# Optimization experiments

Measured on AMD Instinct MI355X. Metric: run time of the kernel, lower is better.

The kernel has to match this reference:

```python
import jax, jax.numpy as jnp
import numpy as np


def setup_inputs() -> dict:
    key = jax.random.key(0)
    k1, k2, k3, k4 = jax.random.split(key, 4)
    B, C, H, W = 16, 256, 128, 128
    HID = 256
    in_feat_map = jax.random.normal(k1, (B, C, H, W), dtype=jnp.float32)
    act_mask = jax.random.randint(k2, (B, 1, H, W), 0, 2).astype(jnp.bool_)
    W1 = jax.random.normal(k3, (C, HID), dtype=jnp.float32) * (1.0 / np.sqrt(C))
    b1 = jnp.zeros((HID,), dtype=jnp.float32)
    W2 = jax.random.normal(k4, (HID, C), dtype=jnp.float32) * (1.0 / np.sqrt(HID))
    b2 = jnp.zeros((C,), dtype=jnp.float32)
    return {"in_feat_map": in_feat_map, "act_mask": act_mask,
            "W1": W1, "b1": b1, "W2": W2, "b2": b2}


def reference(in_feat_map, act_mask, W1, b1, W2, b2):
    # act_mask: [B,1,H,W] -> [B,H,W]. Original gathers active positions,
    # runs a pointwise MLP on [num_act, C] features, scatters back into a
    # clone. Since the inner module is pointwise per position, this equals
    # computing the MLP everywhere and selecting with the mask (same math,
    # static shapes, jit-friendly).
    mask = act_mask[:, 0]  # [B,H,W]
    # per-position 2-layer MLP over channel dim
    h = jnp.einsum('bchw,cd->bdhw', in_feat_map, W1) + b1[None, :, None, None]
    h = jax.nn.relu(h)
    y = jnp.einsum('bdhw,dc->bchw', h, W2) + b2[None, :, None, None]
    out_feat_map = jnp.where(mask[:, None, :, :], y, in_feat_map)
    return out_feat_map
```

## Files before the change

kernel.cpp:

```cpp
#include <hip/hip_runtime.h>

typedef _Float16 h4 __attribute__((ext_vector_type(4)));
typedef _Float16 h8 __attribute__((ext_vector_type(8)));
typedef float f4 __attribute__((ext_vector_type(4)));

#define CIN 256
#define HID 256
#define HWSZ 16384
#define NT 64

__global__ __launch_bounds__(256) void wconv_kernel(const float* __restrict__ W1,
                                                    const float* __restrict__ W2,
                                                    _Float16* __restrict__ W1f,
                                                    _Float16* __restrict__ W2f) {
  int t = blockIdx.x * 256 + threadIdx.x;
  int m = t & 255;
  int k = t >> 8;
  int fi = ((k >> 5) << 13) | ((m >> 4) << 9) | (((k >> 3) & 3) << 7) |
           ((m & 15) << 3) | (k & 7);
  W1f[fi] = (_Float16)W1[k * 256 + m];
  W2f[fi] = (_Float16)W2[k * 256 + m];
}

__global__ __launch_bounds__(256, 2) void mlp_kernel(
    const float* __restrict__ in, const int* __restrict__ mask,
    const float* __restrict__ b1, const float* __restrict__ b2,
    const _Float16* __restrict__ W1f, const _Float16* __restrict__ W2f,
    float* __restrict__ out) {
  __shared__ alignas(16) _Float16 Xs[NT * 256];
  __shared__ alignas(16) _Float16 Hs[NT * 256];

  const int t = threadIdx.x;
  const int g = blockIdx.x;
  const int b = g >> 8;
  const int hw0 = (g & 255) * NT;
  const float* inb = in + (size_t)b * CIN * HWSZ + hw0;

  {
    const int n = t & 63;
    const int cg = (t >> 6) * 4;
    const int sw = (n & 7) << 3;
#pragma unroll
    for (int i = 0; i < 16; ++i) {
      const int c0 = i * 16 + cg;
      float x0 = inb[(size_t)(c0 + 0) * HWSZ + n];
      float x1 = inb[(size_t)(c0 + 1) * HWSZ + n];
      float x2 = inb[(size_t)(c0 + 2) * HWSZ + n];
      float x3 = inb[(size_t)(c0 + 3) * HWSZ + n];
      h4 xv;
      xv[0] = (_Float16)x0; xv[1] = (_Float16)x1;
      xv[2] = (_Float16)x2; xv[3] = (_Float16)x3;
      *(h4*)&Xs[n * 256 + (c0 ^ sw)] = xv;
    }
  }
  __syncthreads();

  const int w = t >> 6;
  const int l = t & 63;
  const int li = l & 15;
  const int q = l >> 4;

  f4 acc[4][4];
#pragma unroll
  for (int mt = 0; mt < 4; ++mt)
#pragma unroll
    for (int nt = 0; nt < 4; ++nt)
#pragma unroll
      for (int r = 0; r < 4; ++r) acc[mt][nt][r] = 0.f;

#pragma unroll 2
  for (int kc = 0; kc < 8; ++kc) {
    h8 af[4], bf[4];
#pragma unroll
    for (int mt = 0; mt < 4; ++mt)
      af[mt] = *(const h8*)(W1f + (kc << 13) + ((4 * w + mt) << 9) + (l << 3));
#pragma unroll
    for (int nt = 0; nt < 4; ++nt) {
      const int nn = nt * 16 + li;
      bf[nt] = *(const h8*)&Xs[nn * 256 + (((kc << 5) + (q << 3)) ^ ((nn & 7) << 3))];
    }
#pragma unroll
    for (int mt = 0; mt < 4; ++mt)
#pragma unroll
      for (int nt = 0; nt < 4; ++nt)
        acc[mt][nt] = __builtin_amdgcn_mfma_f32_16x16x32_f16(af[mt], bf[nt], acc[mt][nt], 0, 0, 0);
  }

#pragma unroll
  for (int mt = 0; mt < 4; ++mt) {
    const int d0 = w * 64 + mt * 16 + q * 4;
    const f4 bb = *(const f4*)(b1 + d0);
#pragma unroll
    for (int nt = 0; nt < 4; ++nt) {
      const int nn = nt * 16 + li;
      h4 hv;
#pragma unroll
      for (int r = 0; r < 4; ++r) {
        float v = acc[mt][nt][r] + bb[r];
        hv[r] = (_Float16)(v > 0.f ? v : 0.f);
      }
      *(h4*)&Hs[nn * 256 + (d0 ^ ((nn & 7) << 3))] = hv;
    }
  }
  __syncthreads();

#pragma unroll
  for (int mt = 0; mt < 4; ++mt)
#pragma unroll
    for (int nt = 0; nt < 4; ++nt)
#pragma unroll
      for (int r = 0; r < 4; ++r) acc[mt][nt][r] = 0.f;

#pragma unroll 2
  for (int kc = 0; kc < 8; ++kc) {
    h8 af[4], bf[4];
#pragma unroll
    for (int mt = 0; mt < 4; ++mt)
      af[mt] = *(const h8*)(W2f + (kc << 13) + ((4 * w + mt) << 9) + (l << 3));
#pragma unroll
    for (int nt = 0; nt < 4; ++nt) {
      const int nn = nt * 16 + li;
      bf[nt] = *(const h8*)&Hs[nn * 256 + (((kc << 5) + (q << 3)) ^ ((nn & 7) << 3))];
    }
#pragma unroll
    for (int mt = 0; mt < 4; ++mt)
#pragma unroll
      for (int nt = 0; nt < 4; ++nt)
        acc[mt][nt] = __builtin_amdgcn_mfma_f32_16x16x32_f16(af[mt], bf[nt], acc[mt][nt], 0, 0, 0);
  }

  const int* mb = mask + b * HWSZ + hw0;
  int mv[4];
#pragma unroll
  for (int nt = 0; nt < 4; ++nt) mv[nt] = mb[nt * 16 + li];

  float* outb = out + (size_t)b * CIN * HWSZ + hw0;
#pragma unroll
  for (int ct = 0; ct < 4; ++ct) {
    const int c0 = w * 64 + ct * 16 + q * 4;
    const f4 bb = *(const f4*)(b2 + c0);
#pragma unroll
    for (int nt = 0; nt < 4; ++nt) {
      const int nn = nt * 16 + li;
      const h4 xv = *(const h4*)&Xs[nn * 256 + (c0 ^ ((nn & 7) << 3))];
#pragma unroll
      for (int r = 0; r < 4; ++r) {
        float y = acc[ct][nt][r] + bb[r];
        outb[(size_t)(c0 + r) * HWSZ + nn] = mv[nt] ? y : (float)xv[r];
      }
    }
  }
}

extern "C" void kernel_launch(void* const* d_in, const int* in_sizes, int n_in,
                              void* d_out, int out_size, void* d_ws, size_t ws_size,
                              hipStream_t stream) {
  const float* in = (const float*)d_in[0];
  const int* mask = (const int*)d_in[1];
  const float* W1 = (const float*)d_in[2];
  const float* b1 = (const float*)d_in[3];
  const float* W2 = (const float*)d_in[4];
  const float* b2 = (const float*)d_in[5];
  float* out = (float*)d_out;

  _Float16* W1f = (_Float16*)d_ws;
  _Float16* W2f = W1f + 65536;

  hipLaunchKernelGGL(wconv_kernel, dim3(256), dim3(256), 0, stream, W1, W2, W1f, W2f);
  hipLaunchKernelGGL(mlp_kernel, dim3(16 * (HWSZ / NT)), dim3(256), 0, stream,
                     in, mask, b1, b2, W1f, W2f, out);
}
```

Before: 514.2 us.

## Share one LDS buffer, transpose second GEMM, vectorize epilogue with fp32 passthrough

Merges the X and H shared-memory tiles into one buffer, adding a barrier before H overwrites X. This halves LDS per block so four blocks per CU can be resident. The second GEMM swaps operand roles so the accumulator is laid out position-major, which allows 16-byte vector stores and mask loads. Unmasked positions now re-read the original fp32 input from global memory instead of the fp16 copy, which restores exact passthrough at the cost of extra global reads.

```diff
diff --git a/kernel.cpp b/kernel.cpp
--- a/kernel.cpp
+++ b/kernel.cpp
@@ -3,6 +3,7 @@
 typedef _Float16 h4 __attribute__((ext_vector_type(4)));
 typedef _Float16 h8 __attribute__((ext_vector_type(8)));
 typedef float f4 __attribute__((ext_vector_type(4)));
+typedef int i4 __attribute__((ext_vector_type(4)));
 
 #define CIN 256
 #define HID 256
@@ -22,13 +23,12 @@
   W2f[fi] = (_Float16)W2[k * 256 + m];
 }
 
-__global__ __launch_bounds__(256, 2) void mlp_kernel(
+__global__ __launch_bounds__(256, 4) void mlp_kernel(
     const float* __restrict__ in, const int* __restrict__ mask,
     const float* __restrict__ b1, const float* __restrict__ b2,
     const _Float16* __restrict__ W1f, const _Float16* __restrict__ W2f,
     float* __restrict__ out) {
-  __shared__ alignas(16) _Float16 Xs[NT * 256];
-  __shared__ alignas(16) _Float16 Hs[NT * 256];
+  __shared__ alignas(16) _Float16 S[NT * 256];
 
   const int t = threadIdx.x;
   const int g = blockIdx.x;
@@ -50,7 +50,7 @@
       h4 xv;
       xv[0] = (_Float16)x0; xv[1] = (_Float16)x1;
       xv[2] = (_Float16)x2; xv[3] = (_Float16)x3;
-      *(h4*)&Xs[n * 256 + (c0 ^ sw)] = xv;
+      *(h4*)&S[n * 256 + (c0 ^ sw)] = xv;
     }
   }
   __syncthreads();
@@ -59,6 +59,7 @@
   const int l = t & 63;
   const int li = l & 15;
   const int q = l >> 4;
+  const int swl = (li & 7) << 3;
 
   f4 acc[4][4];
 #pragma unroll
@@ -75,16 +76,15 @@
     for (int mt = 0; mt < 4; ++mt)
       af[mt] = *(const h8*)(W1f + (kc << 13) + ((4 * w + mt) << 9) + (l << 3));
 #pragma unroll
-    for (int nt = 0; nt < 4; ++nt) {
-      const int nn = nt * 16 + li;
-      bf[nt] = *(const h8*)&Xs[nn * 256 + (((kc << 5) + (q << 3)) ^ ((nn & 7) << 3))];
-    }
+    for (int nt = 0; nt < 4; ++nt)
+      bf[nt] = *(const h8*)&S[(nt * 16 + li) * 256 + (((kc << 5) + (q << 3)) ^ swl)];
 #pragma unroll
     for (int mt = 0; mt < 4; ++mt)
 #pragma unroll
       for (int nt = 0; nt < 4; ++nt)
         acc[mt][nt] = __builtin_amdgcn_mfma_f32_16x16x32_f16(af[mt], bf[nt], acc[mt][nt], 0, 0, 0);
   }
+  __syncthreads();
 
 #pragma unroll
   for (int mt = 0; mt < 4; ++mt) {
@@ -99,7 +99,7 @@
         float v = acc[mt][nt][r] + bb[r];
         hv[r] = (_Float16)(v > 0.f ? v : 0.f);
       }
-      *(h4*)&Hs[nn * 256 + (d0 ^ ((nn & 7) << 3))] = hv;
+      *(h4*)&S[nn * 256 + (d0 ^ swl)] = hv;
     }
   }
   __syncthreads();
@@ -116,12 +116,10 @@
     h8 af[4], bf[4];
 #pragma unroll
     for (int mt = 0; mt < 4; ++mt)
-      af[mt] = *(const h8*)(W2f + (kc << 13) + ((4 * w + mt) << 9) + (l << 3));
+      af[mt] = *(const h8*)&S[(mt * 16 + li) * 256 + (((kc << 5) + (q << 3)) ^ swl)];
 #pragma unroll
-    for (int nt = 0; nt < 4; ++nt) {
-      const int nn = nt * 16 + li;
-      bf[nt] = *(const h8*)&Hs[nn * 256 + (((kc << 5) + (q << 3)) ^ ((nn & 7) << 3))];
-    }
+    for (int nt = 0; nt < 4; ++nt)
+      bf[nt] = *(const h8*)(W2f + (kc << 13) + ((4 * w + nt) << 9) + (l << 3));
 #pragma unroll
     for (int mt = 0; mt < 4; ++mt)
 #pragma unroll
@@ -130,24 +128,31 @@
   }
 
   const int* mb = mask + b * HWSZ + hw0;
-  int mv[4];
+  i4 m4[4];
 #pragma unroll
-  for (int nt = 0; nt < 4; ++nt) mv[nt] = mb[nt * 16 + li];
+  for (int mt = 0; mt < 4; ++mt) m4[mt] = *(const i4*)&mb[mt * 16 + q * 4];
+  float b2v[4];
+#pragma unroll
+  for (int nt = 0; nt < 4; ++nt) b2v[nt] = b2[w * 64 + nt * 16 + li];
 
   float* outb = out + (size_t)b * CIN * HWSZ + hw0;
 #pragma unroll
-  for (int ct = 0; ct < 4; ++ct) {
-    const int c0 = w * 64 + ct * 16 + q * 4;
-    const f4 bb = *(const f4*)(b2 + c0);
+  for (int mt = 0; mt < 4; ++mt) {
+    const int n0 = mt * 16 + q * 4;
+    f4 xv[4];
 #pragma unroll
     for (int nt = 0; nt < 4; ++nt) {
-      const int nn = nt * 16 + li;
-      const h4 xv = *(const h4*)&Xs[nn * 256 + (c0 ^ ((nn & 7) << 3))];
+      const size_t off = (size_t)(w * 64 + nt * 16 + li) * HWSZ + n0;
+      xv[nt] = *(const f4*)&inb[off];
+    }
 #pragma unroll
-      for (int r = 0; r < 4; ++r) {
-        float y = acc[ct][nt][r] + bb[r];
-        outb[(size_t)(c0 + r) * HWSZ + nn] = mv[nt] ? y : (float)xv[r];
-      }
+    for (int nt = 0; nt < 4; ++nt) {
+      const size_t off = (size_t)(w * 64 + nt * 16 + li) * HWSZ + n0;
+      f4 y;
+#pragma unroll
+      for (int r = 0; r < 4; ++r)
+        y[r] = m4[mt][r] ? (acc[mt][nt][r] + b2v[nt]) : xv[nt][r];
+      *(f4*)&outb[off] = y;
     }
   }
 }
```

New measurement: 528.4 us. 2.8% more time.
